# Kernel tuning notes

Measured on AMD Instinct MI355X. Metric: run time of the kernel, lower is better.

Reference implementation:

```python
import jax, jax.numpy as jnp
import numpy as np

N = 50000      # nodes
D = 128        # in_dim
O = 128        # out_dim
MAX_DEG = 32   # degrees uniform in [0, MAX_DEG]


def setup_inputs() -> dict:
    rng = np.random.default_rng(0)
    deg = rng.integers(0, MAX_DEG + 1, size=N)          # includes deg==0 nodes
    dst = np.repeat(np.arange(N), deg)                  # target node per edge (grouped, like the buckets)
    E = dst.shape[0]                                    # ~800000
    src = rng.integers(0, N, size=E)                    # neighbor index per edge (flat neighbor_list)

    key = jax.random.key(0)
    k1, k2, k3, k4 = jax.random.split(key, 4)
    scale = jnp.float32(1.0 / np.sqrt(D))
    return {
        "x":  jax.random.normal(k1, (N, D), jnp.float32),
        "Wg": jax.random.normal(k2, (O, D), jnp.float32) * scale,  # global_lin.weight
        "Wl": jax.random.normal(k3, (O, D), jnp.float32) * scale,  # local_lin.weight
        "Ws": jax.random.normal(k4, (O, D), jnp.float32) * scale,  # self_lin.weight
        "b":  jnp.zeros((O,), jnp.float32),                        # bias param
        "src": jnp.asarray(src, jnp.int32),
        "dst": jnp.asarray(dst, jnp.int32),
        "deg": jnp.asarray(deg, jnp.int32),
    }


def reference(x, Wg, Wl, Ws, b, src, dst, deg):
    n = x.shape[0]
    # global branch: applied to every node
    g_out = x @ Wg.T                                           # [N, O]
    # mean-aggregate neighbor features (gather + segment-sum == the per-bucket view().mean())
    neigh_sum = jax.ops.segment_sum(x[src], dst, num_segments=n)   # [N, D]
    degf = jnp.maximum(deg, 1).astype(x.dtype)[:, None]
    neigh_mean = neigh_sum * (1.0 / degf)                       # [N, D]
    # local + self branches only for deg > 0 (deg==0 bucket keeps just global_out)
    mask = (deg > 0).astype(x.dtype)[:, None]                   # [N, 1]
    out = g_out + mask * (neigh_mean @ Wl.T + x @ Ws.T) + b
    # dropout is identity in eval mode; ELU activation
    return jax.nn.elu(out)
```

## Files before the change

### kernel.cpp

```cpp
#include <hip/hip_runtime.h>
#include <cstdint>
#include <cstddef>

#define D_IN   128
#define O_DIM  128
#define KCAT   384
#define BM     64
#define BK     32
#define AGG_BLOCK 512
#define AGG_NPB   8

typedef __attribute__((ext_vector_type(8))) short bf16x8;
typedef __attribute__((ext_vector_type(4))) float f32x4;

static __device__ __forceinline__ unsigned short f2bf(float f) {
    unsigned int u = __builtin_bit_cast(unsigned int, f);
    unsigned int lsb = (u >> 16) & 1u;
    u += 0x7fffu + lsb;
    return (unsigned short)(u >> 16);
}
static __device__ __forceinline__ float bfhi(unsigned int u) {
    return __builtin_bit_cast(float, u & 0xFFFF0000u);
}
static __device__ __forceinline__ float bflo(unsigned int u) {
    return __builtin_bit_cast(float, u << 16);
}

static __device__ __forceinline__ void async16(const unsigned short* g, void* lds_wave_base) {
    __builtin_amdgcn_global_load_lds(
        (const __attribute__((address_space(1))) void*)g,
        (__attribute__((address_space(3))) void*)lds_wave_base,
        16, 0, 0);
}

__global__ void build_V(const float* __restrict__ Wg, const float* __restrict__ Wl,
                        const float* __restrict__ Ws, unsigned short* __restrict__ V) {
    const int o = blockIdx.x;
    const int k = threadIdx.x;
    float v;
    if (k < 128)      v = Wg[o * 128 + k];
    else if (k < 256) v = Wl[o * 128 + (k - 128)];
    else              v = Ws[o * 128 + (k - 256)];
    V[o * KCAT + k] = f2bf(v);
}

__global__ __launch_bounds__(256)
void convert_x(const float* __restrict__ x, const int* __restrict__ deg,
               unsigned short* __restrict__ xb, unsigned short* __restrict__ zb, int total8) {
    int gid = blockIdx.x * 256 + threadIdx.x;
    if (gid >= total8) return;
    int n = gid >> 4;
    const float4* px = (const float4*)x + (size_t)gid * 2;
    float4 a = px[0], bq = px[1];
    uint4 u;
    u.x = (unsigned)f2bf(a.x)  | ((unsigned)f2bf(a.y)  << 16);
    u.y = (unsigned)f2bf(a.z)  | ((unsigned)f2bf(a.w)  << 16);
    u.z = (unsigned)f2bf(bq.x) | ((unsigned)f2bf(bq.y) << 16);
    u.w = (unsigned)f2bf(bq.z) | ((unsigned)f2bf(bq.w) << 16);
    ((uint4*)xb)[gid] = u;
    uint4 z = u;
    if (deg[n] == 0) { z.x = 0; z.y = 0; z.z = 0; z.w = 0; }
    ((uint4*)zb)[gid] = z;
}

__global__ __launch_bounds__(AGG_BLOCK)
void aggregate(const unsigned short* __restrict__ xb, const int* __restrict__ src,
               const int* __restrict__ dst, const int* __restrict__ deg,
               unsigned short* __restrict__ M, int N, int E) {
    __shared__ int sdeg[AGG_NPB];
    __shared__ int sstart[AGG_NPB];
    const int t    = threadIdx.x;
    const int wv   = t >> 6;
    const int lane = t & 63;
    const int c    = lane & 15;
    const int p    = lane >> 4;
    const int base = blockIdx.x * AGG_NPB;

    if (t < AGG_NPB) {
        int n = base + t;
        sdeg[t] = (n < N) ? deg[n] : 0;
    }
    int lo = 0, hi = E;
    while (lo < hi) {
        int mid = (lo + hi) >> 1;
        if (dst[mid] < base) lo = mid + 1; else hi = mid;
    }
    __syncthreads();
    if (t == 0) {
        int run = lo;
        for (int i = 0; i < AGG_NPB; ++i) { sstart[i] = run; run += sdeg[i]; }
    }
    __syncthreads();

    const int n = base + wv;
    if (n >= N) return;
    const int s = sstart[wv];
    const int d = sdeg[wv];

    int idx = 0;
    if (lane < d) idx = src[s + lane];

    float a[8] = {0,0,0,0,0,0,0,0};
    float b[8] = {0,0,0,0,0,0,0,0};
    const uint4* x4 = (const uint4*)xb;

    for (int g = 0; g * 16 < d; ++g) {
        int e0 = g * 16 + p;
        int r0 = __shfl(idx, e0);
        int r1 = __shfl(idx, e0 + 4);
        int r2 = __shfl(idx, e0 + 8);
        int r3 = __shfl(idx, e0 + 12);
        uint4 v0 = x4[(size_t)r0 * 16 + c];
        uint4 v1 = x4[(size_t)r1 * 16 + c];
        uint4 v2 = x4[(size_t)r2 * 16 + c];
        uint4 v3 = x4[(size_t)r3 * 16 + c];
        if (e0 < d) {
            a[0]+=bflo(v0.x); a[1]+=bfhi(v0.x); a[2]+=bflo(v0.y); a[3]+=bfhi(v0.y);
            a[4]+=bflo(v0.z); a[5]+=bfhi(v0.z); a[6]+=bflo(v0.w); a[7]+=bfhi(v0.w);
        }
        if (e0 + 4 < d) {
            b[0]+=bflo(v1.x); b[1]+=bfhi(v1.x); b[2]+=bflo(v1.y); b[3]+=bfhi(v1.y);
            b[4]+=bflo(v1.z); b[5]+=bfhi(v1.z); b[6]+=bflo(v1.w); b[7]+=bfhi(v1.w);
        }
        if (e0 + 8 < d) {
            a[0]+=bflo(v2.x); a[1]+=bfhi(v2.x); a[2]+=bflo(v2.y); a[3]+=bfhi(v2.y);
            a[4]+=bflo(v2.z); a[5]+=bfhi(v2.z); a[6]+=bflo(v2.w); a[7]+=bfhi(v2.w);
        }
        if (e0 + 12 < d) {
            b[0]+=bflo(v3.x); b[1]+=bfhi(v3.x); b[2]+=bflo(v3.y); b[3]+=bfhi(v3.y);
            b[4]+=bflo(v3.z); b[5]+=bfhi(v3.z); b[6]+=bflo(v3.w); b[7]+=bfhi(v3.w);
        }
    }
#pragma unroll
    for (int i = 0; i < 8; ++i) a[i] += b[i];
#pragma unroll
    for (int i = 0; i < 8; ++i) {
        a[i] += __shfl_xor(a[i], 16, 64);
        a[i] += __shfl_xor(a[i], 32, 64);
    }
    if (p == 0) {
        float inv = (d > 0) ? 1.0f / (float)d : 0.0f;
        uint4 u;
        u.x = (unsigned)f2bf(a[0]*inv) | ((unsigned)f2bf(a[1]*inv) << 16);
        u.y = (unsigned)f2bf(a[2]*inv) | ((unsigned)f2bf(a[3]*inv) << 16);
        u.z = (unsigned)f2bf(a[4]*inv) | ((unsigned)f2bf(a[5]*inv) << 16);
        u.w = (unsigned)f2bf(a[6]*inv) | ((unsigned)f2bf(a[7]*inv) << 16);
        ((uint4*)M)[(size_t)n * 16 + c] = u;
    }
}

__global__ __launch_bounds__(256)
void gemm_epilogue(const unsigned short* __restrict__ xb, const unsigned short* __restrict__ Mm,
                   const unsigned short* __restrict__ zb, const unsigned short* __restrict__ V,
                   const float* __restrict__ bias, float* __restrict__ out, int N) {
    __shared__ __align__(16) unsigned short As[BM * BK];
    __shared__ __align__(16) unsigned short Bs[O_DIM * BK];
    const int t    = threadIdx.x;
    const int w    = t >> 6;
    const int lane = t & 63;
    const int row0 = blockIdx.x * BM;
    const int wcol = w * 32;
    const int quad = lane >> 4;

    f32x4 acc[4][2];
#pragma unroll
    for (int i = 0; i < 4; ++i)
#pragma unroll
        for (int j = 0; j < 2; ++j)
            acc[i][j] = (f32x4){0.f, 0.f, 0.f, 0.f};

    for (int k0 = 0; k0 < KCAT; k0 += BK) {
        const unsigned short* Asrc; int kloc;
        if (k0 < 128)      { Asrc = xb; kloc = k0; }
        else if (k0 < 256) { Asrc = Mm; kloc = k0 - 128; }
        else               { Asrc = zb; kloc = k0 - 256; }

        {
            int row = t >> 2, c4 = t & 3;
            int grow = row0 + row; if (grow > N - 1) grow = N - 1;
            async16(Asrc + (size_t)grow * 128 + kloc + c4 * 8,
                    (char*)As + (size_t)(w * 64) * 16);
        }
#pragma unroll
        for (int it = 0; it < 2; ++it) {
            int f = it * 256 + t;
            int row = f >> 2, c4 = f & 3;
            async16(V + (size_t)row * KCAT + k0 + c4 * 8,
                    (char*)Bs + (size_t)(it * 256 + w * 64) * 16);
        }
        __syncthreads();

        bf16x8 af[4], bfr[2];
#pragma unroll
        for (int ri = 0; ri < 4; ++ri) {
            int rr = ri * 16 + (lane & 15);
            af[ri] = *(const bf16x8*)((const char*)As + rr * 64 + quad * 16);
        }
#pragma unroll
        for (int ci = 0; ci < 2; ++ci) {
            int cc = wcol + ci * 16 + (lane & 15);
            bfr[ci] = *(const bf16x8*)((const char*)Bs + cc * 64 + quad * 16);
        }
#pragma unroll
        for (int ri = 0; ri < 4; ++ri)
#pragma unroll
            for (int ci = 0; ci < 2; ++ci)
                acc[ri][ci] = __builtin_amdgcn_mfma_f32_16x16x32_bf16(af[ri], bfr[ci], acc[ri][ci], 0, 0, 0);
        __syncthreads();
    }

#pragma unroll
    for (int ri = 0; ri < 4; ++ri) {
#pragma unroll
        for (int ci = 0; ci < 2; ++ci) {
            int col = wcol + ci * 16 + (lane & 15);
            float bv = bias[col];
#pragma unroll
            for (int reg = 0; reg < 4; ++reg) {
                int row = row0 + ri * 16 + quad * 4 + reg;
                if (row < N) {
                    float v = acc[ri][ci][reg] + bv;
                    out[(size_t)row * O_DIM + col] = (v > 0.f) ? v : expm1f(v);
                }
            }
        }
    }
}

extern "C" void kernel_launch(void* const* d_in, const int* in_sizes, int n_in,
                              void* d_out, int out_size, void* d_ws, size_t ws_size,
                              hipStream_t stream) {
    const float* x  = (const float*)d_in[0];
    const float* Wg = (const float*)d_in[1];
    const float* Wl = (const float*)d_in[2];
    const float* Ws = (const float*)d_in[3];
    const float* b  = (const float*)d_in[4];
    const int*   src = (const int*)d_in[5];
    const int*   dst = (const int*)d_in[6];
    const int*   deg = (const int*)d_in[7];
    const int E = in_sizes[5];
    const int N = in_sizes[7];
    float* out = (float*)d_out;

    const size_t NB = (size_t)N * 128 * 2;
    unsigned short* V  = (unsigned short*)d_ws;
    unsigned short* xb = (unsigned short*)((char*)d_ws + 98304);
    unsigned short* Mm = (unsigned short*)((char*)d_ws + 98304 + NB);
    unsigned short* zb = (unsigned short*)((char*)d_ws + 98304 + 2 * NB);

    build_V<<<dim3(O_DIM), dim3(KCAT), 0, stream>>>(Wg, Wl, Ws, V);
    int total8 = N * 16;
    convert_x<<<dim3((total8 + 255) / 256), dim3(256), 0, stream>>>(x, deg, xb, zb, total8);
    aggregate<<<dim3((N + AGG_NPB - 1) / AGG_NPB), dim3(AGG_BLOCK), 0, stream>>>(xb, src, dst, deg, Mm, N, E);
    gemm_epilogue<<<dim3((N + BM - 1) / BM), dim3(256), 0, stream>>>(xb, Mm, zb, V, b, out, N);
}
```

Before: 159.4 us.

## Fuse neighbor aggregation into GEMM via LDS-resident concatenated A tile

Merges the aggregate and GEMM kernels. Each 512-thread block gathers and averages neighbors for 64 nodes and writes the [x | mean | masked x] row straight into padded LDS, so the Mm and zb intermediate buffers are no longer written to and reread from global memory. The B operand (V) is read directly from global memory with a one-step register prefetch instead of being staged in LDS, and the per-block start offsets come from a wave-level prefix scan. In exchange the MFMA phase cannot start until the whole block's gather finishes, and the large LDS footprint (about 50 KB per block) may reduce occupancy.

```diff
diff --git a/kernel.cpp b/kernel.cpp
--- a/kernel.cpp
+++ b/kernel.cpp
@@ -2,13 +2,9 @@
 #include <cstdint>
 #include <cstddef>
 
-#define D_IN   128
-#define O_DIM  128
-#define KCAT   384
-#define BM     64
-#define BK     32
-#define AGG_BLOCK 512
-#define AGG_NPB   8
+#define KCAT  384
+#define AST   392
+#define NPB   64
 
 typedef __attribute__((ext_vector_type(8))) short bf16x8;
 typedef __attribute__((ext_vector_type(4))) float f32x4;
@@ -25,12 +21,9 @@
 static __device__ __forceinline__ float bflo(unsigned int u) {
     return __builtin_bit_cast(float, u << 16);
 }
-
-static __device__ __forceinline__ void async16(const unsigned short* g, void* lds_wave_base) {
-    __builtin_amdgcn_global_load_lds(
-        (const __attribute__((address_space(1))) void*)g,
-        (__attribute__((address_space(3))) void*)lds_wave_base,
-        16, 0, 0);
+static __device__ __forceinline__ void acc8(float* a, const uint4& v) {
+    a[0] += bflo(v.x); a[1] += bfhi(v.x); a[2] += bflo(v.y); a[3] += bfhi(v.y);
+    a[4] += bflo(v.z); a[5] += bfhi(v.z); a[6] += bflo(v.w); a[7] += bfhi(v.w);
 }
 
 __global__ void build_V(const float* __restrict__ Wg, const float* __restrict__ Wl,
@@ -45,11 +38,9 @@
 }
 
 __global__ __launch_bounds__(256)
-void convert_x(const float* __restrict__ x, const int* __restrict__ deg,
-               unsigned short* __restrict__ xb, unsigned short* __restrict__ zb, int total8) {
+void convert_x(const float* __restrict__ x, unsigned short* __restrict__ xb, int total8) {
     int gid = blockIdx.x * 256 + threadIdx.x;
     if (gid >= total8) return;
-    int n = gid >> 4;
     const float4* px = (const float4*)x + (size_t)gid * 2;
     float4 a = px[0], bq = px[1];
     uint4 u;
@@ -58,169 +49,131 @@
     u.z = (unsigned)f2bf(bq.x) | ((unsigned)f2bf(bq.y) << 16);
     u.w = (unsigned)f2bf(bq.z) | ((unsigned)f2bf(bq.w) << 16);
     ((uint4*)xb)[gid] = u;
-    uint4 z = u;
-    if (deg[n] == 0) { z.x = 0; z.y = 0; z.z = 0; z.w = 0; }
-    ((uint4*)zb)[gid] = z;
-}
-
-__global__ __launch_bounds__(AGG_BLOCK)
-void aggregate(const unsigned short* __restrict__ xb, const int* __restrict__ src,
-               const int* __restrict__ dst, const int* __restrict__ deg,
-               unsigned short* __restrict__ M, int N, int E) {
-    __shared__ int sdeg[AGG_NPB];
-    __shared__ int sstart[AGG_NPB];
+}
+
+__global__ __launch_bounds__(512, 6)
+void fused_agg_gemm(const unsigned short* __restrict__ xb, const int* __restrict__ src,
+                    const int* __restrict__ dst, const int* __restrict__ deg,
+                    const unsigned short* __restrict__ V, const float* __restrict__ bias,
+                    float* __restrict__ out, int N, int E) {
+    __shared__ __align__(16) unsigned short Ash[NPB * AST];
+    __shared__ int sstart[NPB];
+    __shared__ int sdeg[NPB];
     const int t    = threadIdx.x;
     const int wv   = t >> 6;
     const int lane = t & 63;
     const int c    = lane & 15;
     const int p    = lane >> 4;
-    const int base = blockIdx.x * AGG_NPB;
-
-    if (t < AGG_NPB) {
-        int n = base + t;
-        sdeg[t] = (n < N) ? deg[n] : 0;
-    }
-    int lo = 0, hi = E;
-    while (lo < hi) {
-        int mid = (lo + hi) >> 1;
-        if (dst[mid] < base) lo = mid + 1; else hi = mid;
+    const int base = blockIdx.x * NPB;
+
+    if (wv == 0) {
+        int lo = 0, hi = E;
+        while (lo < hi) { int mid = (lo + hi) >> 1; if (dst[mid] < base) lo = mid + 1; else hi = mid; }
+        int n  = base + lane;
+        int dg = (n < N) ? deg[n] : 0;
+        int incl = dg;
+#pragma unroll
+        for (int off = 1; off < 64; off <<= 1) {
+            int v = __shfl_up(incl, off, 64);
+            if (lane >= off) incl += v;
+        }
+        sstart[lane] = lo + incl - dg;
+        sdeg[lane]   = dg;
     }
     __syncthreads();
-    if (t == 0) {
-        int run = lo;
-        for (int i = 0; i < AGG_NPB; ++i) { sstart[i] = run; run += sdeg[i]; }
+
+    const uint4* x4 = (const uint4*)xb;
+    for (int r = 0; r < 8; ++r) {
+        const int row = wv * 8 + r;
+        const int n   = base + row;
+        const int d   = sdeg[row];
+        const int s   = sstart[row];
+        int idx = 0;
+        if (lane < d) idx = src[s + lane];
+        uint4 xv = {0, 0, 0, 0};
+        if (p == 1 && n < N) xv = x4[(size_t)n * 16 + c];
+
+        float a[8] = {0,0,0,0,0,0,0,0};
+        float b[8] = {0,0,0,0,0,0,0,0};
+        for (int g = 0; g * 16 < d; ++g) {
+            int e0 = g * 16 + p;
+            int r0 = __shfl(idx, e0, 64);
+            int r1 = __shfl(idx, e0 + 4, 64);
+            int r2 = __shfl(idx, e0 + 8, 64);
+            int r3 = __shfl(idx, e0 + 12, 64);
+            uint4 v0 = x4[(size_t)r0 * 16 + c];
+            uint4 v1 = x4[(size_t)r1 * 16 + c];
+            uint4 v2 = x4[(size_t)r2 * 16 + c];
+            uint4 v3 = x4[(size_t)r3 * 16 + c];
+            if (e0 < d)      acc8(a, v0);
+            if (e0 + 4 < d)  acc8(b, v1);
+            if (e0 + 8 < d)  acc8(a, v2);
+            if (e0 + 12 < d) acc8(b, v3);
+        }
+#pragma unroll
+        for (int i = 0; i < 8; ++i) a[i] += b[i];
+#pragma unroll
+        for (int i = 0; i < 8; ++i) {
+            a[i] += __shfl_xor(a[i], 16, 64);
+            a[i] += __shfl_xor(a[i], 32, 64);
+        }
+        unsigned short* arow = Ash + row * AST;
+        if (p == 0) {
+            float inv = (d > 0) ? 1.0f / (float)d : 0.0f;
+            uint4 u;
+            u.x = (unsigned)f2bf(a[0]*inv) | ((unsigned)f2bf(a[1]*inv) << 16);
+            u.y = (unsigned)f2bf(a[2]*inv) | ((unsigned)f2bf(a[3]*inv) << 16);
+            u.z = (unsigned)f2bf(a[4]*inv) | ((unsigned)f2bf(a[5]*inv) << 16);
+            u.w = (unsigned)f2bf(a[6]*inv) | ((unsigned)f2bf(a[7]*inv) << 16);
+            *(uint4*)(arow + 128 + c * 8) = u;
+        } else if (p == 1) {
+            *(uint4*)(arow + c * 8) = xv;
+            uint4 z = xv;
+            if (d == 0) { z.x = 0; z.y = 0; z.z = 0; z.w = 0; }
+            *(uint4*)(arow + 256 + c * 8) = z;
+        }
     }
     __syncthreads();
 
-    const int n = base + wv;
-    if (n >= N) return;
-    const int s = sstart[wv];
-    const int d = sdeg[wv];
-
-    int idx = 0;
-    if (lane < d) idx = src[s + lane];
-
-    float a[8] = {0,0,0,0,0,0,0,0};
-    float b[8] = {0,0,0,0,0,0,0,0};
-    const uint4* x4 = (const uint4*)xb;
-
-    for (int g = 0; g * 16 < d; ++g) {
-        int e0 = g * 16 + p;
-        int r0 = __shfl(idx, e0);
-        int r1 = __shfl(idx, e0 + 4);
-        int r2 = __shfl(idx, e0 + 8);
-        int r3 = __shfl(idx, e0 + 12);
-        uint4 v0 = x4[(size_t)r0 * 16 + c];
-        uint4 v1 = x4[(size_t)r1 * 16 + c];
-        uint4 v2 = x4[(size_t)r2 * 16 + c];
-        uint4 v3 = x4[(size_t)r3 * 16 + c];
-        if (e0 < d) {
-            a[0]+=bflo(v0.x); a[1]+=bfhi(v0.x); a[2]+=bflo(v0.y); a[3]+=bfhi(v0.y);
-            a[4]+=bflo(v0.z); a[5]+=bfhi(v0.z); a[6]+=bflo(v0.w); a[7]+=bfhi(v0.w);
-        }
-        if (e0 + 4 < d) {
-            b[0]+=bflo(v1.x); b[1]+=bfhi(v1.x); b[2]+=bflo(v1.y); b[3]+=bfhi(v1.y);
-            b[4]+=bflo(v1.z); b[5]+=bfhi(v1.z); b[6]+=bflo(v1.w); b[7]+=bfhi(v1.w);
-        }
-        if (e0 + 8 < d) {
-            a[0]+=bflo(v2.x); a[1]+=bfhi(v2.x); a[2]+=bflo(v2.y); a[3]+=bfhi(v2.y);
-            a[4]+=bflo(v2.z); a[5]+=bfhi(v2.z); a[6]+=bflo(v2.w); a[7]+=bfhi(v2.w);
-        }
-        if (e0 + 12 < d) {
-            b[0]+=bflo(v3.x); b[1]+=bfhi(v3.x); b[2]+=bflo(v3.y); b[3]+=bfhi(v3.y);
-            b[4]+=bflo(v3.z); b[5]+=bfhi(v3.z); b[6]+=bflo(v3.w); b[7]+=bfhi(v3.w);
-        }
-    }
-#pragma unroll
-    for (int i = 0; i < 8; ++i) a[i] += b[i];
-#pragma unroll
-    for (int i = 0; i < 8; ++i) {
-        a[i] += __shfl_xor(a[i], 16, 64);
-        a[i] += __shfl_xor(a[i], 32, 64);
-    }
-    if (p == 0) {
-        float inv = (d > 0) ? 1.0f / (float)d : 0.0f;
-        uint4 u;
-        u.x = (unsigned)f2bf(a[0]*inv) | ((unsigned)f2bf(a[1]*inv) << 16);
-        u.y = (unsigned)f2bf(a[2]*inv) | ((unsigned)f2bf(a[3]*inv) << 16);
-        u.z = (unsigned)f2bf(a[4]*inv) | ((unsigned)f2bf(a[5]*inv) << 16);
-        u.w = (unsigned)f2bf(a[6]*inv) | ((unsigned)f2bf(a[7]*inv) << 16);
-        ((uint4*)M)[(size_t)n * 16 + c] = u;
-    }
-}
-
-__global__ __launch_bounds__(256)
-void gemm_epilogue(const unsigned short* __restrict__ xb, const unsigned short* __restrict__ Mm,
-                   const unsigned short* __restrict__ zb, const unsigned short* __restrict__ V,
-                   const float* __restrict__ bias, float* __restrict__ out, int N) {
-    __shared__ __align__(16) unsigned short As[BM * BK];
-    __shared__ __align__(16) unsigned short Bs[O_DIM * BK];
-    const int t    = threadIdx.x;
-    const int w    = t >> 6;
-    const int lane = t & 63;
-    const int row0 = blockIdx.x * BM;
-    const int wcol = w * 32;
+    const int wrow = (wv >> 2) * 32;
+    const int wcol = (wv & 3) * 32;
     const int quad = lane >> 4;
-
-    f32x4 acc[4][2];
-#pragma unroll
-    for (int i = 0; i < 4; ++i)
-#pragma unroll
-        for (int j = 0; j < 2; ++j)
-            acc[i][j] = (f32x4){0.f, 0.f, 0.f, 0.f};
-
-    for (int k0 = 0; k0 < KCAT; k0 += BK) {
-        const unsigned short* Asrc; int kloc;
-        if (k0 < 128)      { Asrc = xb; kloc = k0; }
-        else if (k0 < 256) { Asrc = Mm; kloc = k0 - 128; }
-        else               { Asrc = zb; kloc = k0 - 256; }
-
-        {
-            int row = t >> 2, c4 = t & 3;
-            int grow = row0 + row; if (grow > N - 1) grow = N - 1;
-            async16(Asrc + (size_t)grow * 128 + kloc + c4 * 8,
-                    (char*)As + (size_t)(w * 64) * 16);
-        }
-#pragma unroll
-        for (int it = 0; it < 2; ++it) {
-            int f = it * 256 + t;
-            int row = f >> 2, c4 = f & 3;
-            async16(V + (size_t)row * KCAT + k0 + c4 * 8,
-                    (char*)Bs + (size_t)(it * 256 + w * 64) * 16);
-        }
-        __syncthreads();
-
-        bf16x8 af[4], bfr[2];
-#pragma unroll
-        for (int ri = 0; ri < 4; ++ri) {
-            int rr = ri * 16 + (lane & 15);
-            af[ri] = *(const bf16x8*)((const char*)As + rr * 64 + quad * 16);
-        }
+    const unsigned short* V0 = V + (size_t)(wcol + c) * KCAT + quad * 8;
+    const unsigned short* V1 = V + (size_t)(wcol + 16 + c) * KCAT + quad * 8;
+
+    f32x4 acc[2][2];
+#pragma unroll
+    for (int i = 0; i < 2; ++i)
+#pragma unroll
+        for (int j = 0; j < 2; ++j) acc[i][j] = (f32x4){0.f, 0.f, 0.f, 0.f};
+
+    bf16x8 b0 = *(const bf16x8*)V0;
+    bf16x8 b1 = *(const bf16x8*)V1;
+    for (int k0 = 0; k0 < KCAT; k0 += 32) {
+        int kn = (k0 + 32 < KCAT) ? k0 + 32 : 0;
+        bf16x8 n0 = *(const bf16x8*)(V0 + kn);
+        bf16x8 n1 = *(const bf16x8*)(V1 + kn);
+        bf16x8 a0 = *(const bf16x8*)(Ash + (size_t)(wrow + c) * AST + k0 + quad * 8);
+        bf16x8 a1 = *(const bf16x8*)(Ash + (size_t)(wrow + 16 + c) * AST + k0 + quad * 8);
+        acc[0][0] = __builtin_amdgcn_mfma_f32_16x16x32_bf16(a0, b0, acc[0][0], 0, 0, 0);
+        acc[0][1] = __builtin_amdgcn_mfma_f32_16x16x32_bf16(a0, b1, acc[0][1], 0, 0, 0);
+        acc[1][0] = __builtin_amdgcn_mfma_f32_16x16x32_bf16(a1, b0, acc[1][0], 0, 0, 0);
+        acc[1][1] = __builtin_amdgcn_mfma_f32_16x16x32_bf16(a1, b1, acc[1][1], 0, 0, 0);
+        b0 = n0; b1 = n1;
+    }
+
+#pragma unroll
+    for (int ri = 0; ri < 2; ++ri) {
 #pragma unroll
         for (int ci = 0; ci < 2; ++ci) {
-            int cc = wcol + ci * 16 + (lane & 15);
-            bfr[ci] = *(const bf16x8*)((const char*)Bs + cc * 64 + quad * 16);
-        }
-#pragma unroll
-        for (int ri = 0; ri < 4; ++ri)
-#pragma unroll
-            for (int ci = 0; ci < 2; ++ci)
-                acc[ri][ci] = __builtin_amdgcn_mfma_f32_16x16x32_bf16(af[ri], bfr[ci], acc[ri][ci], 0, 0, 0);
-        __syncthreads();
-    }
-
-#pragma unroll
-    for (int ri = 0; ri < 4; ++ri) {
-#pragma unroll
-        for (int ci = 0; ci < 2; ++ci) {
-            int col = wcol + ci * 16 + (lane & 15);
+            int col = wcol + ci * 16 + c;
             float bv = bias[col];
 #pragma unroll
             for (int reg = 0; reg < 4; ++reg) {
-                int row = row0 + ri * 16 + quad * 4 + reg;
-                if (row < N) {
+                int grow = base + wrow + ri * 16 + quad * 4 + reg;
+                if (grow < N) {
                     float v = acc[ri][ci][reg] + bv;
-                    out[(size_t)row * O_DIM + col] = (v > 0.f) ? v : expm1f(v);
+                    out[(size_t)grow * 128 + col] = (v > 0.f) ? v : expm1f(v);
                 }
             }
         }
@@ -242,15 +195,12 @@
     const int N = in_sizes[7];
     float* out = (float*)d_out;
 
-    const size_t NB = (size_t)N * 128 * 2;
     unsigned short* V  = (unsigned short*)d_ws;
     unsigned short* xb = (unsigned short*)((char*)d_ws + 98304);
-    unsigned short* Mm = (unsigned short*)((char*)d_ws + 98304 + NB);
-    unsigned short* zb = (unsigned short*)((char*)d_ws + 98304 + 2 * NB);
-
-    build_V<<<dim3(O_DIM), dim3(KCAT), 0, stream>>>(Wg, Wl, Ws, V);
+
+    build_V<<<dim3(128), dim3(KCAT), 0, stream>>>(Wg, Wl, Ws, V);
     int total8 = N * 16;
-    convert_x<<<dim3((total8 + 255) / 256), dim3(256), 0, stream>>>(x, deg, xb, zb, total8);
-    aggregate<<<dim3((N + AGG_NPB - 1) / AGG_NPB), dim3(AGG_BLOCK), 0, stream>>>(xb, src, dst, deg, Mm, N, E);
-    gemm_epilogue<<<dim3((N + BM - 1) / BM), dim3(256), 0, stream>>>(xb, Mm, zb, V, b, out, N);
-}
+    convert_x<<<dim3((total8 + 255) / 256), dim3(256), 0, stream>>>(x, xb, total8);
+    fused_agg_gemm<<<dim3((N + NPB - 1) / NPB), dim3(512), 0, stream>>>(
+        xb, src, dst, deg, V, b, out, N, E);
+}
```

After: 160.5 us. Within noise of the previous version (+0.7%).
